# Optimization experiments

Measured on AMD Instinct MI355X. Metric: run time of the kernel, lower is better.

Reference implementation:

```python
import jax, jax.numpy as jnp
import numpy as np

N = 768  # length of time vector

def setup_inputs() -> dict:
    key = jax.random.key(0)
    ks = jax.random.split(key, 4)
    # time vector (sorted grid-like values, as in a GP time axis)
    x = jnp.sort(jax.random.uniform(ks[0], (N,), dtype=jnp.float32) * (6 * np.pi))
    # MLP params: Linear(2,1024) -> Sigmoid -> Linear(1024,128) -> ReLU -> Linear(128,1)
    W1 = jax.random.normal(ks[1], (1024, 2), dtype=jnp.float32) * (1.0 / np.sqrt(2.0))
    b1 = jnp.zeros((1024,), dtype=jnp.float32)
    W2 = jax.random.normal(ks[2], (128, 1024), dtype=jnp.float32) * (1.0 / np.sqrt(1024.0))
    b2 = jnp.zeros((128,), dtype=jnp.float32)
    W3 = jax.random.normal(ks[3], (1, 128), dtype=jnp.float32) * (1.0 / np.sqrt(128.0))
    b3 = jnp.zeros((1,), dtype=jnp.float32)
    return {"x": x, "W1": W1, "b1": b1, "W2": W2, "b2": b2, "W3": W3, "b3": b3}


def reference(x, W1, b1, W2, b2, W3, b3):
    n = x.shape[0]
    # all (i, j) with j >= i  -> n(n+1)/2 pairs; replaces the Python double loop
    iu, ju = jnp.triu_indices(n)
    pairs = jnp.stack([x[iu], x[ju]], axis=-1)            # [P, 2]
    h = jax.nn.sigmoid(pairs @ W1.T + b1)                 # [P, 1024]
    h = jax.nn.relu(h @ W2.T + b2)                        # [P, 128]
    v = (h @ W3.T + b3)[:, 0]                             # [P]
    # K starts as eye; upper triangle INCLUDING diagonal is overwritten
    K = jnp.eye(n, dtype=x.dtype).at[iu, ju].set(v)       # [n, n] upper-triangular
    return K.T @ K                                        # symmetric PSD covariance
```

## Files before the change

kernel.cpp:

```cpp
#include <hip/hip_runtime.h>
#include <hip/hip_bf16.h>

#define NN 768
#define MD 1024
#define NPAIR 295296
#define NPBLK2 2307

typedef __attribute__((ext_vector_type(8))) short s16x8;
typedef __attribute__((ext_vector_type(4))) float f32x4;
typedef __attribute__((ext_vector_type(2))) __bf16 b16x2;

__device__ __forceinline__ ushort bf16_rn(float f) {
    uint u = __builtin_bit_cast(uint, f);
    u += 0x7FFFu + ((u >> 16) & 1u);
    return (ushort)(u >> 16);
}

__device__ __forceinline__ void ptoij(int p, int& io, int& jo) {
    const float disc = (float)(1537 * 1537 - 8 * p);
    int i = (int)((1537.0f - sqrtf(disc)) * 0.5f);
    i = i < 0 ? 0 : (i > 767 ? 767 : i);
    while (i > 0 && p < i * (1537 - i) / 2) --i;
    while (i < 767 && p >= (i + 1) * (1536 - i) / 2) ++i;
    io = i;
    jo = i + (p - i * (1537 - i) / 2);
}

#define GLOAD16(gsrc, ldst)                                                        \
    __builtin_amdgcn_global_load_lds(                                              \
        (const __attribute__((address_space(1))) void*)(gsrc),                     \
        (__attribute__((address_space(3))) void*)(ldst), 16, 0, 0)

__global__ __launch_bounds__(256) void w2bf16(const float* __restrict__ W2,
                                              ushort* __restrict__ WhiS)
{
    const int id = blockIdx.x * 256 + threadIdx.x;
    const int k = id >> 7;
    const int m = (id & 127) * 8;
    const float4 a = *reinterpret_cast<const float4*>(W2 + k * MD + m);
    const float4 b = *reinterpret_cast<const float4*>(W2 + k * MD + m + 4);
    const float w[8] = {a.x, a.y, a.z, a.w, b.x, b.y, b.z, b.w};
    s16x8 h;
#pragma unroll
    for (int e = 0; e < 8; ++e) h[e] = (short)bf16_rn(w[e]);
    const int c = m >> 6;
    const int mloc8 = (m >> 3) & 7;
    const int byte = (mloc8 * 16) ^ ((k & 7) << 4);
    const int off = c * 8192 + ((k * 128 + byte) >> 1);
    *reinterpret_cast<s16x8*>(&WhiS[off]) = h;
}

#define STAGE(cc, buf)                                                       \
    {                                                                        \
        const ushort* sh_ = WhiS + (cc) * 8192;                              \
        _Pragma("unroll")                                                    \
        for (int q_ = 0; q_ < 4; ++q_) {                                     \
            const int off_ = (wv * 4 + q_) * 512;                            \
            GLOAD16(sh_ + off_ + lane * 8, &Wh[buf][off_]);                  \
        }                                                                    \
    }

#define SIG_CHUNK(cc, dst, TMN)                                              \
    {                                                                        \
        _Pragma("unroll")                                                    \
        for (int ks_ = 0; ks_ < 2; ++ks_) {                                  \
            const int m0_ = (cc) * 64 + ks_ * 32 + l4 * 8;                   \
            const f32x4 a0_ = *reinterpret_cast<const f32x4*>(&sa[m0_]);     \
            const f32x4 a1_ = *reinterpret_cast<const f32x4*>(&sa[m0_ + 4]); \
            const f32x4 c0_ = *reinterpret_cast<const f32x4*>(&sc[m0_]);     \
            const f32x4 c1_ = *reinterpret_cast<const f32x4*>(&sc[m0_ + 4]); \
            const f32x4 b0_ = *reinterpret_cast<const f32x4*>(&sb[m0_]);     \
            const f32x4 b1_ = *reinterpret_cast<const f32x4*>(&sb[m0_ + 4]); \
            _Pragma("unroll")                                                \
            for (int tm_ = 0; tm_ < (TMN); ++tm_) {                          \
                float s_[8];                                                 \
                _Pragma("unroll")                                            \
                for (int e_ = 0; e_ < 4; ++e_) {                             \
                    const float u0_ = fmaf(xia[tm_], a0_[e_], fmaf(xja[tm_], c0_[e_], b0_[e_])); \
                    const float u1_ = fmaf(xia[tm_], a1_[e_], fmaf(xja[tm_], c1_[e_], b1_[e_])); \
                    s_[e_]     = __builtin_amdgcn_rcpf(1.0f + __builtin_amdgcn_exp2f(u0_)); \
                    s_[e_ + 4] = __builtin_amdgcn_rcpf(1.0f + __builtin_amdgcn_exp2f(u1_)); \
                }                                                            \
                union { s16x8 v; uint u[4]; } fr_;                           \
                _Pragma("unroll")                                            \
                for (int h_ = 0; h_ < 4; ++h_) {                             \
                    b16x2 p_;                                                \
                    p_.x = (__bf16)s_[2 * h_];                               \
                    p_.y = (__bf16)s_[2 * h_ + 1];                           \
                    fr_.u[h_] = __builtin_bit_cast(uint, p_);                \
                }                                                            \
                dst[ks_][tm_] = fr_.v;                                       \
            }                                                                \
        }                                                                    \
    }

#define MFMA_STEP(buf, src, TMN)                                             \
    {                                                                        \
        _Pragma("unroll")                                                    \
        for (int ks_ = 0; ks_ < 2; ++ks_) {                                  \
            _Pragma("unroll")                                                \
            for (int th_ = 0; th_ < 2; ++th_) {                              \
                s16x8 bh_[4];                                                \
                _Pragma("unroll")                                            \
                for (int tn_ = 0; tn_ < 4; ++tn_) {                          \
                    const int k_ = th_ * 64 + tn_ * 16 + l15;                \
                    const int byte_ = (ks_ * 64 + l4 * 16) ^ ((k_ & 7) << 4);\
                    const int idx_ = (k_ * 128 + byte_) >> 1;                \
                    bh_[tn_] = *reinterpret_cast<const s16x8*>(&Wh[buf][idx_]); \
                }                                                            \
                __builtin_amdgcn_s_setprio(1);                               \
                _Pragma("unroll")                                            \
                for (int tm_ = 0; tm_ < (TMN); ++tm_)                        \
                    _Pragma("unroll")                                        \
                    for (int tn_ = 0; tn_ < 4; ++tn_)                        \
                        acc[tm_][th_][tn_] = __builtin_amdgcn_mfma_f32_16x16x32_bf16( \
                            src[ks_][tm_], bh_[tn_], acc[tm_][th_][tn_], 0, 0, 0);    \
                __builtin_amdgcn_s_setprio(0);                               \
            }                                                                \
        }                                                                    \
    }

__global__ __launch_bounds__(256, 3) void mlp_pairs(
    const float* __restrict__ x,
    const float* __restrict__ W1, const float* __restrict__ b1,
    const ushort* __restrict__ WhiS,
    const float* __restrict__ b2, const float* __restrict__ W3,
    const float* __restrict__ b3, float* __restrict__ K)
{
    __shared__ __align__(16) float sa[MD], sc[MD], sb[MD];
    __shared__ __align__(16) ushort Wh[2][8192];

    const int t = threadIdx.x;
    const int lane = t & 63, wv = t >> 6;
    const int l15 = lane & 15, l4 = lane >> 4;

    const float NL2E = -1.4426950408889634f;
    for (int m = t; m < MD; m += 256) {
        const float2 w = reinterpret_cast<const float2*>(W1)[m];
        sa[m] = w.x * NL2E;
        sc[m] = w.y * NL2E;
        sb[m] = b1[m] * NL2E;
    }

    const int pairbase = blockIdx.x * 128 + wv * 32;

    float xia[2], xja[2];
#pragma unroll
    for (int tm = 0; tm < 2; ++tm) {
        const int p = pairbase + tm * 16 + l15;
        if (p < NPAIR) {
            int i, j;
            ptoij(p, i, j);
            xia[tm] = x[i];
            xja[tm] = x[j];
        } else {
            xia[tm] = 0.f;
            xja[tm] = 0.f;
        }
    }

    f32x4 acc[2][2][4];
#pragma unroll
    for (int a = 0; a < 2; ++a)
#pragma unroll
        for (int th = 0; th < 2; ++th)
#pragma unroll
            for (int b = 0; b < 4; ++b) acc[a][th][b] = (f32x4){0.f, 0.f, 0.f, 0.f};

    STAGE(0, 0);
    __syncthreads();

    s16x8 ah[2][2];
    for (int c = 0; c < 16; ++c) {
        if (c < 15) STAGE(c + 1, (c + 1) & 1);
        SIG_CHUNK(c, ah, 2);
        MFMA_STEP(c & 1, ah, 2);
        __syncthreads();
    }

    float w3v[2][4], b2v[2][4];
#pragma unroll
    for (int th = 0; th < 2; ++th)
#pragma unroll
        for (int tn = 0; tn < 4; ++tn) {
            const int k = th * 64 + tn * 16 + l15;
            w3v[th][tn] = W3[k];
            b2v[th][tn] = b2[k];
        }
    const float b3v = b3[0];
#pragma unroll
    for (int tm = 0; tm < 2; ++tm)
#pragma unroll
        for (int r = 0; r < 4; ++r) {
            float v = 0.f;
#pragma unroll
            for (int th = 0; th < 2; ++th)
#pragma unroll
                for (int tn = 0; tn < 4; ++tn)
                    v = fmaf(w3v[th][tn], fmaxf(acc[tm][th][tn][r] + b2v[th][tn], 0.f), v);
            v += __shfl_xor(v, 1, 16);
            v += __shfl_xor(v, 2, 16);
            v += __shfl_xor(v, 4, 16);
            v += __shfl_xor(v, 8, 16);
            if (l15 == 0) {
                const int p = pairbase + tm * 16 + l4 * 4 + r;
                if (p < NPAIR) {
                    int i, j;
                    ptoij(p, i, j);
                    K[i * NN + j] = v + b3v;
                }
            }
        }
}

#define MC 32
#define JT 128
#define SPAD 132
__global__ __launch_bounds__(256) void mlp_fill(
    const float* __restrict__ x,
    const float* __restrict__ W1, const float* __restrict__ b1,
    const float* __restrict__ W2, const float* __restrict__ b2,
    const float* __restrict__ W3, const float* __restrict__ b3,
    float* __restrict__ K)
{
    const int i  = blockIdx.y;
    const int j0 = blockIdx.x * JT;
    if (j0 + JT - 1 < i) return;
    __shared__ float sA[MD];
    __shared__ float sCw[MD];
    __shared__ float sxj[JT];
    __shared__ float S[MC][SPAD];
    __shared__ float W2t[MC][SPAD];
    const int t = threadIdx.x;
    const float xi = x[i];
    for (int m = t; m < MD; m += 256) {
        const float2 w = reinterpret_cast<const float2*>(W1)[m];
        sA[m]  = fmaf(xi, w.x, b1[m]);
        sCw[m] = w.y;
    }
    if (t < JT) sxj[t] = x[j0 + t];
    const int tk = t & 15;
    const int tj = t >> 4;
    float w3r[8], b2r[8];
#pragma unroll
    for (int kk = 0; kk < 8; kk++) {
        w3r[kk] = W3[tk * 8 + kk];
        b2r[kk] = b2[tk * 8 + kk];
    }
    float acc[8][8];
#pragma unroll
    for (int jj = 0; jj < 8; jj++)
#pragma unroll
        for (int kk = 0; kk < 8; kk++) acc[jj][kk] = 0.f;
    const int jx   = t & 127;
    const int mseg = (t >> 7) * 16;
    __syncthreads();
    const float xjv = sxj[jx];
    for (int m0 = 0; m0 < MD; m0 += MC) {
#pragma unroll
        for (int q = 0; q < 4; q++) {
            const int f   = t + q * 256;
            const int k   = f >> 3;
            const int mm4 = (f & 7) * 4;
            const float4 w = *reinterpret_cast<const float4*>(W2 + k * MD + m0 + mm4);
            W2t[mm4 + 0][k] = w.x;
            W2t[mm4 + 1][k] = w.y;
            W2t[mm4 + 2][k] = w.z;
            W2t[mm4 + 3][k] = w.w;
        }
#pragma unroll
        for (int q = 0; q < 16; q++) {
            const int ml = mseg + q;
            const float z = fmaf(xjv, sCw[m0 + ml], sA[m0 + ml]);
            S[ml][jx] = 1.0f / (1.0f + __expf(-z));
        }
        __syncthreads();
#pragma unroll 4
        for (int mm = 0; mm < MC; mm++) {
            const float4 s0 = *reinterpret_cast<const float4*>(&S[mm][tj * 8]);
            const float4 s1 = *reinterpret_cast<const float4*>(&S[mm][tj * 8 + 4]);
            const float4 w0 = *reinterpret_cast<const float4*>(&W2t[mm][tk * 8]);
            const float4 w1 = *reinterpret_cast<const float4*>(&W2t[mm][tk * 8 + 4]);
            const float sj[8] = {s0.x, s0.y, s0.z, s0.w, s1.x, s1.y, s1.z, s1.w};
            const float wk[8] = {w0.x, w0.y, w0.z, w0.w, w1.x, w1.y, w1.z, w1.w};
#pragma unroll
            for (int jj = 0; jj < 8; jj++)
#pragma unroll
                for (int kk = 0; kk < 8; kk++)
                    acc[jj][kk] = fmaf(sj[jj], wk[kk], acc[jj][kk]);
        }
        __syncthreads();
    }
    const float b3v = b3[0];
#pragma unroll
    for (int jj = 0; jj < 8; jj++) {
        float v = 0.f;
#pragma unroll
        for (int kk = 0; kk < 8; kk++) {
            const float h = acc[jj][kk] + b2r[kk];
            v = fmaf(w3r[kk], fmaxf(h, 0.f), v);
        }
#pragma unroll
        for (int off = 8; off >= 1; off >>= 1)
            v += __shfl_xor(v, off, 16);
        if (tk == 0) {
            const int j = j0 + tj * 8 + jj;
            if (j >= i) K[i * NN + j] = v + b3v;
        }
    }
}

__global__ __launch_bounds__(256) void ktk(const float* __restrict__ K,
                                           float* __restrict__ C)
{
    const int b0 = blockIdx.x * 64;
    const int a0 = blockIdx.y * 64;
    __shared__ float Ka[64][68];
    __shared__ float Kb[64][68];
    const int t  = threadIdx.x;
    const int tb = t & 15;
    const int ta = t >> 4;
    float acc[4][4];
#pragma unroll
    for (int u = 0; u < 4; u++)
#pragma unroll
        for (int v = 0; v < 4; v++) acc[u][v] = 0.f;
    const int kmax = (a0 < b0 ? a0 : b0) + 64;
    for (int k0 = 0; k0 < kmax; k0 += 64) {
#pragma unroll
        for (int q = 0; q < 4; q++) {
            const int f  = t + q * 256;
            const int kk = f >> 4;
            const int c4 = (f & 15) * 4;
            *reinterpret_cast<float4*>(&Ka[kk][c4]) =
                *reinterpret_cast<const float4*>(K + (k0 + kk) * NN + a0 + c4);
            *reinterpret_cast<float4*>(&Kb[kk][c4]) =
                *reinterpret_cast<const float4*>(K + (k0 + kk) * NN + b0 + c4);
        }
        __syncthreads();
#pragma unroll 8
        for (int kk = 0; kk < 64; kk++) {
            const float4 av = *reinterpret_cast<const float4*>(&Ka[kk][ta * 4]);
            const float4 bv = *reinterpret_cast<const float4*>(&Kb[kk][tb * 4]);
            const float a4[4] = {av.x, av.y, av.z, av.w};
            const float b4[4] = {bv.x, bv.y, bv.z, bv.w};
#pragma unroll
            for (int u = 0; u < 4; u++)
#pragma unroll
                for (int v = 0; v < 4; v++)
                    acc[u][v] = fmaf(a4[u], b4[v], acc[u][v]);
        }
        __syncthreads();
    }
#pragma unroll
    for (int u = 0; u < 4; u++) {
        float4 o;
        o.x = acc[u][0]; o.y = acc[u][1]; o.z = acc[u][2]; o.w = acc[u][3];
        *reinterpret_cast<float4*>(C + (a0 + ta * 4 + u) * NN + b0 + tb * 4) = o;
    }
}

extern "C" void kernel_launch(void* const* d_in, const int* in_sizes, int n_in,
                              void* d_out, int out_size, void* d_ws, size_t ws_size,
                              hipStream_t stream)
{
    const float* x  = (const float*)d_in[0];
    const float* W1 = (const float*)d_in[1];
    const float* b1 = (const float*)d_in[2];
    const float* W2 = (const float*)d_in[3];
    const float* b2 = (const float*)d_in[4];
    const float* W3 = (const float*)d_in[5];
    const float* b3 = (const float*)d_in[6];
    float* Kmat = (float*)d_ws;
    float* C    = (float*)d_out;

    const size_t kBytes = (size_t)NN * NN * sizeof(float);
    const size_t need   = kBytes + 262144;

    hipMemsetAsync(Kmat, 0, kBytes, stream);
    if (ws_size >= need) {
        ushort* WhiS = (ushort*)((char*)d_ws + kBytes);
        w2bf16<<<64, 256, 0, stream>>>(W2, WhiS);
        mlp_pairs<<<NPBLK2, 256, 0, stream>>>(x, W1, b1, WhiS, b2, W3, b3, Kmat);
    } else {
        mlp_fill<<<dim3(6, NN), 256, 0, stream>>>(x, W1, b1, W2, b2, W3, b3, Kmat);
    }
    ktk<<<dim3(NN / 64, NN / 64), 256, 0, stream>>>(Kmat, C);
}
```

Before: 177.4 us.

## Use 512-thread blocks with four-buffer W2 staging and packed sigmoid math

Doubles the block size to 512 threads (8 waves, 256 pairs per block) so each staged W2 chunk in shared memory is shared by twice as many pairs. W2 staging now uses four LDS buffers, loading two chunks at a time and syncing once per two chunks, which halves the barrier count. The sigmoid pre-activation is computed with packed float2 FMAs. The trade-offs are higher LDS use per block (four 16KB buffers), fewer resident blocks, and a different occupancy target of 4 via launch bounds.

```diff
diff --git a/kernel.cpp b/kernel.cpp
--- a/kernel.cpp
+++ b/kernel.cpp
@@ -4,10 +4,11 @@
 #define NN 768
 #define MD 1024
 #define NPAIR 295296
-#define NPBLK2 2307
+#define NPBLK3 1154
 
 typedef __attribute__((ext_vector_type(8))) short s16x8;
 typedef __attribute__((ext_vector_type(4))) float f32x4;
+typedef __attribute__((ext_vector_type(2))) float f32x2;
 typedef __attribute__((ext_vector_type(2))) __bf16 b16x2;
 
 __device__ __forceinline__ ushort bf16_rn(float f) {
@@ -50,17 +51,18 @@
     *reinterpret_cast<s16x8*>(&WhiS[off]) = h;
 }
 
-#define STAGE(cc, buf)                                                       \
+#define STAGE8(cc)                                                           \
     {                                                                        \
         const ushort* sh_ = WhiS + (cc) * 8192;                              \
+        ushort* ld_ = Wh[(cc) & 3];                                          \
         _Pragma("unroll")                                                    \
-        for (int q_ = 0; q_ < 4; ++q_) {                                     \
-            const int off_ = (wv * 4 + q_) * 512;                            \
-            GLOAD16(sh_ + off_ + lane * 8, &Wh[buf][off_]);                  \
+        for (int q_ = 0; q_ < 2; ++q_) {                                     \
+            const int off_ = (wv * 2 + q_) * 512;                            \
+            GLOAD16(sh_ + off_ + lane * 8, ld_ + off_);                      \
         }                                                                    \
     }
 
-#define SIG_CHUNK(cc, dst, TMN)                                              \
+#define SIG_CHUNK(cc, dst)                                                   \
     {                                                                        \
         _Pragma("unroll")                                                    \
         for (int ks_ = 0; ks_ < 2; ++ks_) {                                  \
@@ -72,21 +74,32 @@
             const f32x4 b0_ = *reinterpret_cast<const f32x4*>(&sb[m0_]);     \
             const f32x4 b1_ = *reinterpret_cast<const f32x4*>(&sb[m0_ + 4]); \
             _Pragma("unroll")                                                \
-            for (int tm_ = 0; tm_ < (TMN); ++tm_) {                          \
-                float s_[8];                                                 \
-                _Pragma("unroll")                                            \
-                for (int e_ = 0; e_ < 4; ++e_) {                             \
-                    const float u0_ = fmaf(xia[tm_], a0_[e_], fmaf(xja[tm_], c0_[e_], b0_[e_])); \
-                    const float u1_ = fmaf(xia[tm_], a1_[e_], fmaf(xja[tm_], c1_[e_], b1_[e_])); \
-                    s_[e_]     = __builtin_amdgcn_rcpf(1.0f + __builtin_amdgcn_exp2f(u0_)); \
-                    s_[e_ + 4] = __builtin_amdgcn_rcpf(1.0f + __builtin_amdgcn_exp2f(u1_)); \
-                }                                                            \
+            for (int tm_ = 0; tm_ < 2; ++tm_) {                              \
+                const f32x2 xi2_ = (f32x2){xia[tm_], xia[tm_]};              \
+                const f32x2 xj2_ = (f32x2){xja[tm_], xja[tm_]};              \
+                const f32x2 one2_ = (f32x2){1.f, 1.f};                       \
                 union { s16x8 v; uint u[4]; } fr_;                           \
                 _Pragma("unroll")                                            \
                 for (int h_ = 0; h_ < 4; ++h_) {                             \
+                    f32x2 av_, cv_, bv_;                                     \
+                    if (h_ < 2) {                                            \
+                        av_ = (f32x2){a0_[2 * h_], a0_[2 * h_ + 1]};         \
+                        cv_ = (f32x2){c0_[2 * h_], c0_[2 * h_ + 1]};         \
+                        bv_ = (f32x2){b0_[2 * h_], b0_[2 * h_ + 1]};         \
+                    } else {                                                 \
+                        av_ = (f32x2){a1_[2 * h_ - 4], a1_[2 * h_ - 3]};     \
+                        cv_ = (f32x2){c1_[2 * h_ - 4], c1_[2 * h_ - 3]};     \
+                        bv_ = (f32x2){b1_[2 * h_ - 4], b1_[2 * h_ - 3]};     \
+                    }                                                        \
+                    const f32x2 u2_ = __builtin_elementwise_fma(             \
+                        xi2_, av_, __builtin_elementwise_fma(xj2_, cv_, bv_));\
+                    f32x2 e2_;                                               \
+                    e2_[0] = __builtin_amdgcn_exp2f(u2_[0]);                 \
+                    e2_[1] = __builtin_amdgcn_exp2f(u2_[1]);                 \
+                    const f32x2 t2_ = e2_ + one2_;                           \
                     b16x2 p_;                                                \
-                    p_.x = (__bf16)s_[2 * h_];                               \
-                    p_.y = (__bf16)s_[2 * h_ + 1];                           \
+                    p_.x = (__bf16)__builtin_amdgcn_rcpf(t2_[0]);            \
+                    p_.y = (__bf16)__builtin_amdgcn_rcpf(t2_[1]);            \
                     fr_.u[h_] = __builtin_bit_cast(uint, p_);                \
                 }                                                            \
                 dst[ks_][tm_] = fr_.v;                                       \
@@ -94,8 +107,9 @@
         }                                                                    \
     }
 
-#define MFMA_STEP(buf, src, TMN)                                             \
+#define MFMA_STEP(cc, src)                                                   \
     {                                                                        \
+        const ushort* wb_ = Wh[(cc) & 3];                                    \
         _Pragma("unroll")                                                    \
         for (int ks_ = 0; ks_ < 2; ++ks_) {                                  \
             _Pragma("unroll")                                                \
@@ -106,11 +120,11 @@
                     const int k_ = th_ * 64 + tn_ * 16 + l15;                \
                     const int byte_ = (ks_ * 64 + l4 * 16) ^ ((k_ & 7) << 4);\
                     const int idx_ = (k_ * 128 + byte_) >> 1;                \
-                    bh_[tn_] = *reinterpret_cast<const s16x8*>(&Wh[buf][idx_]); \
+                    bh_[tn_] = *reinterpret_cast<const s16x8*>(&wb_[idx_]);  \
                 }                                                            \
                 __builtin_amdgcn_s_setprio(1);                               \
                 _Pragma("unroll")                                            \
-                for (int tm_ = 0; tm_ < (TMN); ++tm_)                        \
+                for (int tm_ = 0; tm_ < 2; ++tm_)                            \
                     _Pragma("unroll")                                        \
                     for (int tn_ = 0; tn_ < 4; ++tn_)                        \
                         acc[tm_][th_][tn_] = __builtin_amdgcn_mfma_f32_16x16x32_bf16( \
@@ -120,7 +134,7 @@
         }                                                                    \
     }
 
-__global__ __launch_bounds__(256, 3) void mlp_pairs(
+__global__ __launch_bounds__(512, 4) void mlp_pairs(
     const float* __restrict__ x,
     const float* __restrict__ W1, const float* __restrict__ b1,
     const ushort* __restrict__ WhiS,
@@ -128,21 +142,21 @@
     const float* __restrict__ b3, float* __restrict__ K)
 {
     __shared__ __align__(16) float sa[MD], sc[MD], sb[MD];
-    __shared__ __align__(16) ushort Wh[2][8192];
+    __shared__ __align__(16) ushort Wh[4][8192];
 
     const int t = threadIdx.x;
     const int lane = t & 63, wv = t >> 6;
     const int l15 = lane & 15, l4 = lane >> 4;
 
     const float NL2E = -1.4426950408889634f;
-    for (int m = t; m < MD; m += 256) {
+    for (int m = t; m < MD; m += 512) {
         const float2 w = reinterpret_cast<const float2*>(W1)[m];
         sa[m] = w.x * NL2E;
         sc[m] = w.y * NL2E;
         sb[m] = b1[m] * NL2E;
     }
 
-    const int pairbase = blockIdx.x * 128 + wv * 32;
+    const int pairbase = blockIdx.x * 256 + wv * 32;
 
     float xia[2], xja[2];
 #pragma unroll
@@ -167,14 +181,20 @@
 #pragma unroll
             for (int b = 0; b < 4; ++b) acc[a][th][b] = (f32x4){0.f, 0.f, 0.f, 0.f};
 
-    STAGE(0, 0);
+    STAGE8(0);
+    STAGE8(1);
     __syncthreads();
 
     s16x8 ah[2][2];
-    for (int c = 0; c < 16; ++c) {
-        if (c < 15) STAGE(c + 1, (c + 1) & 1);
-        SIG_CHUNK(c, ah, 2);
-        MFMA_STEP(c & 1, ah, 2);
+    for (int c = 0; c < 16; c += 2) {
+        if (c < 14) {
+            STAGE8(c + 2);
+            STAGE8(c + 3);
+        }
+        SIG_CHUNK(c, ah);
+        MFMA_STEP(c, ah);
+        SIG_CHUNK(c + 1, ah);
+        MFMA_STEP(c + 1, ah);
         __syncthreads();
     }
 
@@ -381,7 +401,7 @@
     if (ws_size >= need) {
         ushort* WhiS = (ushort*)((char*)d_ws + kBytes);
         w2bf16<<<64, 256, 0, stream>>>(W2, WhiS);
-        mlp_pairs<<<NPBLK2, 256, 0, stream>>>(x, W1, b1, WhiS, b2, W3, b3, Kmat);
+        mlp_pairs<<<NPBLK3, 512, 0, stream>>>(x, W1, b1, WhiS, b2, W3, b3, Kmat);
     } else {
         mlp_fill<<<dim3(6, NN), 256, 0, stream>>>(x, W1, b1, W2, b2, W3, b3, Kmat);
     }
```

Result: slower. 222.0 us (+25.2%).

## Shrink pair tile per block, precompute W1 scales, and exploit symmetry in K^T K

Applied to the files above, without the earlier changes.

The MLP kernel now processes 64 pairs per block (16 per wave) instead of 128, doubling the grid. It drops the per-block LDS tables for scaled W1/b1 in favour of a small prep kernel that writes them to global memory, where they are read directly. The sigmoid uses packed 2-wide FMAs, and occupancy is raised to 4 blocks per CU. The K^T K kernel computes only upper-triangle tiles and writes the transposed tile, roughly halving that GEMM's work. The cost is less reuse of each staged W2 chunk, since fewer pairs share it, in exchange for more parallelism and fewer registers.

```diff
diff --git a/kernel.cpp b/kernel.cpp
--- a/kernel.cpp
+++ b/kernel.cpp
@@ -4,10 +4,11 @@
 #define NN 768
 #define MD 1024
 #define NPAIR 295296
-#define NPBLK2 2307
+#define NBLK4 4614
 
 typedef __attribute__((ext_vector_type(8))) short s16x8;
 typedef __attribute__((ext_vector_type(4))) float f32x4;
+typedef __attribute__((ext_vector_type(2))) float f32x2;
 typedef __attribute__((ext_vector_type(2))) __bf16 b16x2;
 
 __device__ __forceinline__ ushort bf16_rn(float f) {
@@ -44,10 +45,24 @@
 #pragma unroll
     for (int e = 0; e < 8; ++e) h[e] = (short)bf16_rn(w[e]);
     const int c = m >> 6;
-    const int mloc8 = (m >> 3) & 7;
-    const int byte = (mloc8 * 16) ^ ((k & 7) << 4);
+    const int mg = (m >> 3) & 7;
+    const int byte = (mg * 16) ^ ((k & 7) << 4);
     const int off = c * 8192 + ((k * 128 + byte) >> 1);
     *reinterpret_cast<s16x8*>(&WhiS[off]) = h;
+}
+
+__global__ __launch_bounds__(256) void prep1(const float* __restrict__ W1,
+                                             const float* __restrict__ b1,
+                                             float* __restrict__ SA,
+                                             float* __restrict__ SC,
+                                             float* __restrict__ SB)
+{
+    const int m = blockIdx.x * 256 + threadIdx.x;
+    const float NL2E = -1.4426950408889634f;
+    const float2 w = reinterpret_cast<const float2*>(W1)[m];
+    SA[m] = w.x * NL2E;
+    SC[m] = w.y * NL2E;
+    SB[m] = b1[m] * NL2E;
 }
 
 #define STAGE(cc, buf)                                                       \
@@ -60,157 +75,129 @@
         }                                                                    \
     }
 
-#define SIG_CHUNK(cc, dst, TMN)                                              \
+#define SIG_CHUNK(cc)                                                        \
     {                                                                        \
         _Pragma("unroll")                                                    \
         for (int ks_ = 0; ks_ < 2; ++ks_) {                                  \
             const int m0_ = (cc) * 64 + ks_ * 32 + l4 * 8;                   \
-            const f32x4 a0_ = *reinterpret_cast<const f32x4*>(&sa[m0_]);     \
-            const f32x4 a1_ = *reinterpret_cast<const f32x4*>(&sa[m0_ + 4]); \
-            const f32x4 c0_ = *reinterpret_cast<const f32x4*>(&sc[m0_]);     \
-            const f32x4 c1_ = *reinterpret_cast<const f32x4*>(&sc[m0_ + 4]); \
-            const f32x4 b0_ = *reinterpret_cast<const f32x4*>(&sb[m0_]);     \
-            const f32x4 b1_ = *reinterpret_cast<const f32x4*>(&sb[m0_ + 4]); \
+            const f32x4 a0_ = *reinterpret_cast<const f32x4*>(SA + m0_);     \
+            const f32x4 a1_ = *reinterpret_cast<const f32x4*>(SA + m0_ + 4); \
+            const f32x4 c0_ = *reinterpret_cast<const f32x4*>(SC + m0_);     \
+            const f32x4 c1_ = *reinterpret_cast<const f32x4*>(SC + m0_ + 4); \
+            const f32x4 b0_ = *reinterpret_cast<const f32x4*>(SB + m0_);     \
+            const f32x4 b1_ = *reinterpret_cast<const f32x4*>(SB + m0_ + 4); \
+            const f32x2 xi2_ = (f32x2){xi, xi};                              \
+            const f32x2 xj2_ = (f32x2){xj, xj};                              \
+            const f32x2 one2_ = (f32x2){1.f, 1.f};                           \
+            union { s16x8 v; uint u[4]; } fr_;                               \
             _Pragma("unroll")                                                \
-            for (int tm_ = 0; tm_ < (TMN); ++tm_) {                          \
-                float s_[8];                                                 \
-                _Pragma("unroll")                                            \
-                for (int e_ = 0; e_ < 4; ++e_) {                             \
-                    const float u0_ = fmaf(xia[tm_], a0_[e_], fmaf(xja[tm_], c0_[e_], b0_[e_])); \
-                    const float u1_ = fmaf(xia[tm_], a1_[e_], fmaf(xja[tm_], c1_[e_], b1_[e_])); \
-                    s_[e_]     = __builtin_amdgcn_rcpf(1.0f + __builtin_amdgcn_exp2f(u0_)); \
-                    s_[e_ + 4] = __builtin_amdgcn_rcpf(1.0f + __builtin_amdgcn_exp2f(u1_)); \
+            for (int h_ = 0; h_ < 4; ++h_) {                                 \
+                f32x2 av_, cv_, bv_;                                         \
+                if (h_ < 2) {                                                \
+                    av_ = (f32x2){a0_[2 * h_], a0_[2 * h_ + 1]};             \
+                    cv_ = (f32x2){c0_[2 * h_], c0_[2 * h_ + 1]};             \
+                    bv_ = (f32x2){b0_[2 * h_], b0_[2 * h_ + 1]};             \
+                } else {                                                     \
+                    av_ = (f32x2){a1_[2 * h_ - 4], a1_[2 * h_ - 3]};         \
+                    cv_ = (f32x2){c1_[2 * h_ - 4], c1_[2 * h_ - 3]};         \
+                    bv_ = (f32x2){b1_[2 * h_ - 4], b1_[2 * h_ - 3]};         \
                 }                                                            \
-                union { s16x8 v; uint u[4]; } fr_;                           \
-                _Pragma("unroll")                                            \
-                for (int h_ = 0; h_ < 4; ++h_) {                             \
-                    b16x2 p_;                                                \
-                    p_.x = (__bf16)s_[2 * h_];                               \
-                    p_.y = (__bf16)s_[2 * h_ + 1];                           \
-                    fr_.u[h_] = __builtin_bit_cast(uint, p_);                \
-                }                                                            \
-                dst[ks_][tm_] = fr_.v;                                       \
+                const f32x2 u2_ = __builtin_elementwise_fma(                 \
+                    xi2_, av_, __builtin_elementwise_fma(xj2_, cv_, bv_));   \
+                f32x2 e2_;                                                   \
+                e2_[0] = __builtin_amdgcn_exp2f(u2_[0]);                     \
+                e2_[1] = __builtin_amdgcn_exp2f(u2_[1]);                     \
+                const f32x2 t2_ = e2_ + one2_;                               \
+                b16x2 p_;                                                    \
+                p_.x = (__bf16)__builtin_amdgcn_rcpf(t2_[0]);                \
+                p_.y = (__bf16)__builtin_amdgcn_rcpf(t2_[1]);                \
+                fr_.u[h_] = __builtin_bit_cast(uint, p_);                    \
             }                                                                \
+            ah[ks_] = fr_.v;                                                 \
         }                                                                    \
     }
 
-#define MFMA_STEP(buf, src, TMN)                                             \
+#define MFMA_STEP(buf)                                                       \
     {                                                                        \
         _Pragma("unroll")                                                    \
         for (int ks_ = 0; ks_ < 2; ++ks_) {                                  \
+            s16x8 bh_[8];                                                    \
             _Pragma("unroll")                                                \
-            for (int th_ = 0; th_ < 2; ++th_) {                              \
-                s16x8 bh_[4];                                                \
-                _Pragma("unroll")                                            \
-                for (int tn_ = 0; tn_ < 4; ++tn_) {                          \
-                    const int k_ = th_ * 64 + tn_ * 16 + l15;                \
-                    const int byte_ = (ks_ * 64 + l4 * 16) ^ ((k_ & 7) << 4);\
-                    const int idx_ = (k_ * 128 + byte_) >> 1;                \
-                    bh_[tn_] = *reinterpret_cast<const s16x8*>(&Wh[buf][idx_]); \
-                }                                                            \
-                __builtin_amdgcn_s_setprio(1);                               \
-                _Pragma("unroll")                                            \
-                for (int tm_ = 0; tm_ < (TMN); ++tm_)                        \
-                    _Pragma("unroll")                                        \
-                    for (int tn_ = 0; tn_ < 4; ++tn_)                        \
-                        acc[tm_][th_][tn_] = __builtin_amdgcn_mfma_f32_16x16x32_bf16( \
-                            src[ks_][tm_], bh_[tn_], acc[tm_][th_][tn_], 0, 0, 0);    \
-                __builtin_amdgcn_s_setprio(0);                               \
+            for (int tn_ = 0; tn_ < 8; ++tn_) {                              \
+                const int k_ = tn_ * 16 + l15;                               \
+                const int byte_ = (ks_ * 64 + l4 * 16) ^ ((k_ & 7) << 4);    \
+                const int idx_ = (k_ * 128 + byte_) >> 1;                    \
+                bh_[tn_] = *reinterpret_cast<const s16x8*>(&Wh[buf][idx_]);  \
             }                                                                \
+            __builtin_amdgcn_s_setprio(1);                                   \
+            _Pragma("unroll")                                                \
+            for (int tn_ = 0; tn_ < 8; ++tn_)                                \
+                acc[tn_] = __builtin_amdgcn_mfma_f32_16x16x32_bf16(          \
+                    ah[ks_], bh_[tn_], acc[tn_], 0, 0, 0);                   \
+            __builtin_amdgcn_s_setprio(0);                                   \
         }                                                                    \
     }
 
-__global__ __launch_bounds__(256, 3) void mlp_pairs(
+__global__ __launch_bounds__(256, 4) void mlp4(
     const float* __restrict__ x,
-    const float* __restrict__ W1, const float* __restrict__ b1,
+    const float* __restrict__ SA, const float* __restrict__ SC,
+    const float* __restrict__ SB,
     const ushort* __restrict__ WhiS,
     const float* __restrict__ b2, const float* __restrict__ W3,
     const float* __restrict__ b3, float* __restrict__ K)
 {
-    __shared__ __align__(16) float sa[MD], sc[MD], sb[MD];
     __shared__ __align__(16) ushort Wh[2][8192];
 
     const int t = threadIdx.x;
     const int lane = t & 63, wv = t >> 6;
     const int l15 = lane & 15, l4 = lane >> 4;
 
-    const float NL2E = -1.4426950408889634f;
-    for (int m = t; m < MD; m += 256) {
-        const float2 w = reinterpret_cast<const float2*>(W1)[m];
-        sa[m] = w.x * NL2E;
-        sc[m] = w.y * NL2E;
-        sb[m] = b1[m] * NL2E;
-    }
-
-    const int pairbase = blockIdx.x * 128 + wv * 32;
-
-    float xia[2], xja[2];
-#pragma unroll
-    for (int tm = 0; tm < 2; ++tm) {
-        const int p = pairbase + tm * 16 + l15;
-        if (p < NPAIR) {
-            int i, j;
-            ptoij(p, i, j);
-            xia[tm] = x[i];
-            xja[tm] = x[j];
-        } else {
-            xia[tm] = 0.f;
-            xja[tm] = 0.f;
-        }
-    }
-
-    f32x4 acc[2][2][4];
-#pragma unroll
-    for (int a = 0; a < 2; ++a)
-#pragma unroll
-        for (int th = 0; th < 2; ++th)
-#pragma unroll
-            for (int b = 0; b < 4; ++b) acc[a][th][b] = (f32x4){0.f, 0.f, 0.f, 0.f};
+    const int pairbase = blockIdx.x * 64 + wv * 16;
+
+    int pi, pj;
+    ptoij(pairbase + l15, pi, pj);
+    const float xi = x[pi];
+    const float xj = x[pj];
+
+    f32x4 acc[8];
+#pragma unroll
+    for (int b = 0; b < 8; ++b) acc[b] = (f32x4){0.f, 0.f, 0.f, 0.f};
 
     STAGE(0, 0);
     __syncthreads();
 
-    s16x8 ah[2][2];
+    s16x8 ah[2];
     for (int c = 0; c < 16; ++c) {
         if (c < 15) STAGE(c + 1, (c + 1) & 1);
-        SIG_CHUNK(c, ah, 2);
-        MFMA_STEP(c & 1, ah, 2);
-        __syncthreads();
-    }
-
-    float w3v[2][4], b2v[2][4];
-#pragma unroll
-    for (int th = 0; th < 2; ++th)
-#pragma unroll
-        for (int tn = 0; tn < 4; ++tn) {
-            const int k = th * 64 + tn * 16 + l15;
-            w3v[th][tn] = W3[k];
-            b2v[th][tn] = b2[k];
-        }
+        SIG_CHUNK(c);
+        MFMA_STEP(c & 1);
+        __syncthreads();
+    }
+
+    float w3v[8], b2v[8];
+#pragma unroll
+    for (int tn = 0; tn < 8; ++tn) {
+        const int k = tn * 16 + l15;
+        w3v[tn] = W3[k];
+        b2v[tn] = b2[k];
+    }
     const float b3v = b3[0];
 #pragma unroll
-    for (int tm = 0; tm < 2; ++tm)
-#pragma unroll
-        for (int r = 0; r < 4; ++r) {
-            float v = 0.f;
-#pragma unroll
-            for (int th = 0; th < 2; ++th)
-#pragma unroll
-                for (int tn = 0; tn < 4; ++tn)
-                    v = fmaf(w3v[th][tn], fmaxf(acc[tm][th][tn][r] + b2v[th][tn], 0.f), v);
-            v += __shfl_xor(v, 1, 16);
-            v += __shfl_xor(v, 2, 16);
-            v += __shfl_xor(v, 4, 16);
-            v += __shfl_xor(v, 8, 16);
-            if (l15 == 0) {
-                const int p = pairbase + tm * 16 + l4 * 4 + r;
-                if (p < NPAIR) {
-                    int i, j;
-                    ptoij(p, i, j);
-                    K[i * NN + j] = v + b3v;
-                }
-            }
-        }
+    for (int r = 0; r < 4; ++r) {
+        float v = 0.f;
+#pragma unroll
+        for (int tn = 0; tn < 8; ++tn)
+            v = fmaf(w3v[tn], fmaxf(acc[tn][r] + b2v[tn], 0.f), v);
+        v += __shfl_xor(v, 1, 16);
+        v += __shfl_xor(v, 2, 16);
+        v += __shfl_xor(v, 4, 16);
+        v += __shfl_xor(v, 8, 16);
+        if (l15 == 0) {
+            int i, j;
+            ptoij(pairbase + l4 * 4 + r, i, j);
+            K[i * NN + j] = v + b3v;
+        }
+    }
 }
 
 #define MC 32
@@ -315,6 +302,7 @@
 {
     const int b0 = blockIdx.x * 64;
     const int a0 = blockIdx.y * 64;
+    if (b0 < a0) return;
     __shared__ float Ka[64][68];
     __shared__ float Kb[64][68];
     const int t  = threadIdx.x;
@@ -325,7 +313,7 @@
     for (int u = 0; u < 4; u++)
 #pragma unroll
         for (int v = 0; v < 4; v++) acc[u][v] = 0.f;
-    const int kmax = (a0 < b0 ? a0 : b0) + 64;
+    const int kmax = a0 + 64;
     for (int k0 = 0; k0 < kmax; k0 += 64) {
 #pragma unroll
         for (int q = 0; q < 4; q++) {
@@ -357,6 +345,14 @@
         float4 o;
         o.x = acc[u][0]; o.y = acc[u][1]; o.z = acc[u][2]; o.w = acc[u][3];
         *reinterpret_cast<float4*>(C + (a0 + ta * 4 + u) * NN + b0 + tb * 4) = o;
+    }
+    if (b0 > a0) {
+#pragma unroll
+        for (int v = 0; v < 4; v++) {
+            float4 o;
+            o.x = acc[0][v]; o.y = acc[1][v]; o.z = acc[2][v]; o.w = acc[3][v];
+            *reinterpret_cast<float4*>(C + (b0 + tb * 4 + v) * NN + a0 + ta * 4) = o;
+        }
     }
 }
 
@@ -375,13 +371,19 @@
     float* C    = (float*)d_out;
 
     const size_t kBytes = (size_t)NN * NN * sizeof(float);
-    const size_t need   = kBytes + 262144;
+    const size_t wBytes = 262144;
+    const size_t pBytes = 3 * MD * sizeof(float);
+    const size_t need   = kBytes + wBytes + pBytes;
 
     hipMemsetAsync(Kmat, 0, kBytes, stream);
     if (ws_size >= need) {
         ushort* WhiS = (ushort*)((char*)d_ws + kBytes);
+        float*  SA   = (float*)((char*)d_ws + kBytes + wBytes);
+        float*  SC   = SA + MD;
+        float*  SB   = SC + MD;
         w2bf16<<<64, 256, 0, stream>>>(W2, WhiS);
-        mlp_pairs<<<NPBLK2, 256, 0, stream>>>(x, W1, b1, WhiS, b2, W3, b3, Kmat);
+        prep1<<<4, 256, 0, stream>>>(W1, b1, SA, SC, SB);
+        mlp4<<<NBLK4, 256, 0, stream>>>(x, SA, SC, SB, WhiS, b2, W3, b3, Kmat);
     } else {
         mlp_fill<<<dim3(6, NN), 256, 0, stream>>>(x, W1, b1, W2, b2, W3, b3, Kmat);
     }
```

Measured after the change: 208.9 us. +17.8%, slower.
